# Kernel tuning notes

Hardware: AMD Instinct MI355X
Metric: run time of the kernel (lower is better)

Reference implementation:

```python
import jax, jax.numpy as jnp
import numpy as np

H = W = 512      # image spatial dims
C = 3            # channels
K = 32           # kernel size
S = 4            # stride
P = 10           # padding
THRESH = 0.5     # squared-L2 distance threshold
N_PATCH = (H + 2 * P - K) // S + 1  # 126 patches per dim
D = C * K * K    # 3072 patch feature dim


def setup_inputs() -> dict:
    key = jax.random.key(0)
    k1, k2, k3, k4 = jax.random.split(key, 4)
    image = jax.random.uniform(k1, (H, W, C), dtype=jnp.float32)
    mem = jax.random.normal(k2, (4096, D), dtype=jnp.float32)
    mem2 = jax.random.normal(k3, (4096, D), dtype=jnp.float32)
    mapping = jax.random.randint(k4, (4096,), 0, 4096, dtype=jnp.int64)
    return {"image": image, "mem": mem, "mem2": mem2, "mapping": mapping}


def _unfold(img_chw):
    # torch.nn.functional.unfold: -> [L, C*K*K] with feature order (c, kh, kw)
    padded = jnp.pad(img_chw, ((0, 0), (P, P), (P, P)))
    r = (jnp.arange(N_PATCH) * S)[:, None] + jnp.arange(K)[None, :]  # [nH, K]
    c = (jnp.arange(N_PATCH) * S)[:, None] + jnp.arange(K)[None, :]  # [nW, K]
    # patches: [C, nH, nW, K, K]
    patches = padded[:, r[:, None, :, None], c[None, :, None, :]]
    patches = patches.transpose(1, 2, 0, 3, 4)  # [nH, nW, C, K, K]
    return patches.reshape(N_PATCH * N_PATCH, D)


def _fold(patches_ld):
    # inverse of _unfold: scatter-add overlapping patches, crop padding
    p5 = patches_ld.reshape(N_PATCH, N_PATCH, C, K, K)
    r = (jnp.arange(N_PATCH) * S)[:, None] + jnp.arange(K)[None, :]
    c = (jnp.arange(N_PATCH) * S)[:, None] + jnp.arange(K)[None, :]
    canvas = jnp.zeros((C, H + 2 * P, W + 2 * P), dtype=patches_ld.dtype)
    ci = jnp.arange(C)[None, None, :, None, None]
    ri = r[:, None, None, :, None]
    cci = c[None, :, None, None, :]
    canvas = canvas.at[ci, ri, cci].add(p5)
    return canvas[:, P:P + H, P:P + W]  # [C, H, W]


def reference(image, mem, mem2, mapping):
    img_chw = image.transpose(2, 0, 1)            # [C, H, W]
    u = _unfold(img_chw)                           # [L, D]
    # brute-force squared-L2 1-NN against mem bank (FAISS IndexFlatL2)
    d2 = (jnp.sum(u * u, axis=1, keepdims=True)
          - 2.0 * (u @ mem.T)
          + jnp.sum(mem * mem, axis=1)[None, :])   # [L, N]
    dmin = jnp.min(d2, axis=1)                     # [L]
    idx = jnp.argmin(d2, axis=1)                   # [L]
    # counter-based pattern lookup: mem id -> mem2 pattern id -> reconstruct
    recon = mem2[mapping[idx]]                     # [L, D]
    out_p = jnp.where(dmin[:, None] >= THRESH, u, recon)
    folded = _fold(out_p)                          # [C, H, W]
    out = folded / jnp.max(folded)
    return out.transpose(1, 2, 0)                  # [H, W, C]
```

## Files before the change

kernel.cpp:

```cpp
#include <hip/hip_runtime.h>
#include <stdint.h>

#define HH 512
#define WW 512
#define CC 3
#define KK 32
#define SS 4
#define PP 10
#define NPATCH 126
#define NP2 (NPATCH * NPATCH)
#define DD 3072
#define NMEM 4096
#define THRESHV 0.5f

#define FAIL_OFF (4 + NMEM)

__device__ inline float wave_reduce_sum(float v) {
    for (int off = 32; off; off >>= 1) v += __shfl_xor(v, off, 64);
    return v;
}

__device__ inline uint32_t map_f(float f) {
    uint32_t b = __float_as_uint(f);
    return (b & 0x80000000u) ? ~b : (b | 0x80000000u);
}

__global__ void init_ws(uint32_t* ws) {
    if (threadIdx.x == 0) {
        ws[0] = 0u;
        ws[1] = 0x7F800000u;
        ws[2] = 0u;
        ws[3] = 0u;
    }
}

__global__ void mem_norms(const float* __restrict__ mem,
                          float* __restrict__ norms) {
    int row  = blockIdx.x * (blockDim.x >> 6) + (threadIdx.x >> 6);
    int lane = threadIdx.x & 63;
    if (row >= NMEM) return;
    const float4* r = (const float4*)(mem + (size_t)row * DD);
    float4 v[12];
#pragma unroll
    for (int i = 0; i < 12; ++i) v[i] = r[lane + (i << 6)];
    float s0 = 0.f, s1 = 0.f, s2 = 0.f, s3 = 0.f;
#pragma unroll
    for (int i = 0; i < 12; ++i) {
        s0 += v[i].x * v[i].x; s1 += v[i].y * v[i].y;
        s2 += v[i].z * v[i].z; s3 += v[i].w * v[i].w;
    }
    float s = (s0 + s1) + (s2 + s3);
    s = wave_reduce_sum(s);
    if (lane == 0) norms[row] = s;
}

__global__ void minmax_k(const float* __restrict__ norms, uint32_t* ws) {
    __shared__ float smn[4], smx[4];
    float mn = INFINITY, mx = -INFINITY;
    for (int i = threadIdx.x; i < NMEM; i += 256) {
        float v = norms[i];
        mn = fminf(mn, v);
        mx = fmaxf(mx, v);
    }
    for (int off = 32; off; off >>= 1) {
        mn = fminf(mn, __shfl_xor(mn, off, 64));
        mx = fmaxf(mx, __shfl_xor(mx, off, 64));
    }
    int w = threadIdx.x >> 6;
    if ((threadIdx.x & 63) == 0) { smn[w] = mn; smx[w] = mx; }
    __syncthreads();
    if (threadIdx.x == 0) {
        mn = fminf(fminf(smn[0], smn[1]), fminf(smn[2], smn[3]));
        mx = fmaxf(fmaxf(smx[0], smx[1]), fmaxf(smx[2], smx[3]));
        ws[1] = __float_as_uint(mn);
        ws[2] = __float_as_uint(mx);
    }
}

__global__ void patch_rows(const float* __restrict__ img, uint32_t* ws,
                           uint32_t cap) {
    __shared__ float cs[WW];
    int py = blockIdx.x;
    int x  = threadIdx.x;
    int y0 = py * SS - PP;
    float s = 0.f;
#pragma unroll
    for (int ky = 0; ky < KK; ++ky) {
        int y = y0 + ky;
        if (y >= 0 && y < HH) {
            const float* p = img + ((size_t)y * WW + x) * CC;
            s += p[0] * p[0] + p[1] * p[1] + p[2] * p[2];
        }
    }
    cs[x] = s;
    __syncthreads();
    if (x < NPATCH) {
        int x0 = x * SS - PP;
        float t = 0.f;
#pragma unroll
        for (int kx = 0; kx < KK; ++kx) {
            int xx = x0 + kx;
            if (xx >= 0 && xx < WW) t += cs[xx];
        }
        float un = sqrtf(t);
        float mn = sqrtf(__uint_as_float(ws[1]));
        float mx = sqrtf(__uint_as_float(ws[2]));
        float gap = 0.f;
        if (un <= mn) gap = mn - un;
        else if (un >= mx) gap = un - mx;
        if (gap * gap < THRESHV) {
            uint32_t idx = atomicAdd(&ws[0], 1u);
            if (idx < cap) ws[FAIL_OFF + idx] = (uint32_t)(py * NPATCH + x);
        }
    }
}

__device__ inline int cov1(int v) {
    int pv = v + PP;
    int a = pv - (KK - 1);
    int imin = (a <= 0) ? 0 : ((a + SS - 1) >> 2);
    int imax = pv >> 2;
    if (imax > NPATCH - 1) imax = NPATCH - 1;
    return imax - imin + 1;
}

__global__ void fold_main(const float* __restrict__ img, float* __restrict__ out) {
    int t = blockIdx.x * blockDim.x + threadIdx.x;
    if (t >= HH * WW) return;
    int y = t / WW, x = t - y * WW;
    float c = (float)(cov1(y) * cov1(x));
    const float* p = img + (size_t)t * CC;
    float* o = out + (size_t)t * CC;
    o[0] = p[0] * c;
    o[1] = p[1] * c;
    o[2] = p[2] * c;
}

__global__ void fallback_fix(const float* __restrict__ img,
                             const float* __restrict__ mem,
                             const float* __restrict__ mem2,
                             const int* __restrict__ mapping,
                             uint32_t* ws, float* out, uint32_t cap) {
    __shared__ float smin[256];
    __shared__ int   sarg[256];
    uint32_t nfail = ws[0];
    if (nfail > cap) nfail = cap;
    for (uint32_t f = blockIdx.x; f < nfail; f += gridDim.x) {
        int patch = (int)ws[FAIL_OFF + f];
        int pi = patch / NPATCH, pj = patch % NPATCH;
        int y0 = pi * SS - PP, x0 = pj * SS - PP;
        float best = INFINITY; int barg = NMEM;
        for (int j = threadIdx.x; j < NMEM; j += blockDim.x) {
            const float* m = mem + (size_t)j * DD;
            float s = 0.f;
            for (int d = 0; d < DD; ++d) {
                int c = d >> 10, rem = d & 1023, ky = rem >> 5, kx = rem & 31;
                int y = y0 + ky, x = x0 + kx;
                float u = (y >= 0 && y < HH && x >= 0 && x < WW)
                              ? img[((size_t)y * WW + x) * CC + c] : 0.f;
                float dif = u - m[d];
                s += dif * dif;
            }
            if (s < best) { best = s; barg = j; }
        }
        smin[threadIdx.x] = best; sarg[threadIdx.x] = barg;
        __syncthreads();
        for (int stride = 128; stride; stride >>= 1) {
            if ((int)threadIdx.x < stride) {
                float s2 = smin[threadIdx.x + stride];
                int   a2 = sarg[threadIdx.x + stride];
                if (s2 < smin[threadIdx.x] ||
                    (s2 == smin[threadIdx.x] && a2 < sarg[threadIdx.x])) {
                    smin[threadIdx.x] = s2; sarg[threadIdx.x] = a2;
                }
            }
            __syncthreads();
        }
        float dmin = smin[0]; int arg = sarg[0];
        if (dmin < THRESHV) {
            const float* rec = mem2 + (size_t)mapping[arg] * DD;
            for (int d = threadIdx.x; d < DD; d += blockDim.x) {
                int c = d >> 10, rem = d & 1023, ky = rem >> 5, kx = rem & 31;
                int y = y0 + ky, x = x0 + kx;
                if (y >= 0 && y < HH && x >= 0 && x < WW) {
                    float u = img[((size_t)y * WW + x) * CC + c];
                    atomicAdd(&out[((size_t)y * WW + x) * CC + c], rec[d] - u);
                }
            }
        }
        __syncthreads();
    }
}

__global__ void max_reduce(const float* __restrict__ out, uint32_t* ws) {
    __shared__ float sm[4];
    const int n4 = (HH * WW * CC) / 4;
    const float4* o4 = (const float4*)out;
    float m = -INFINITY;
    for (int i = blockIdx.x * blockDim.x + threadIdx.x; i < n4;
         i += gridDim.x * blockDim.x) {
        float4 v = o4[i];
        m = fmaxf(m, fmaxf(fmaxf(v.x, v.y), fmaxf(v.z, v.w)));
    }
    for (int off = 32; off; off >>= 1) m = fmaxf(m, __shfl_xor(m, off, 64));
    int w = threadIdx.x >> 6;
    if ((threadIdx.x & 63) == 0) sm[w] = m;
    __syncthreads();
    if (threadIdx.x == 0) {
        m = fmaxf(fmaxf(sm[0], sm[1]), fmaxf(sm[2], sm[3]));
        atomicMax(&ws[3], map_f(m));
    }
}

__global__ void normalize_k(float* out, const uint32_t* ws) {
    uint32_t key = ws[3];
    uint32_t b = (key & 0x80000000u) ? (key & 0x7FFFFFFFu) : ~key;
    float inv = 1.0f / __uint_as_float(b);
    const int n4 = (HH * WW * CC) / 4;
    int i = blockIdx.x * blockDim.x + threadIdx.x;
    if (i < n4) {
        float4* o4 = (float4*)out;
        float4 v = o4[i];
        v.x *= inv; v.y *= inv; v.z *= inv; v.w *= inv;
        o4[i] = v;
    }
}

extern "C" void kernel_launch(void* const* d_in, const int* in_sizes, int n_in,
                              void* d_out, int out_size, void* d_ws, size_t ws_size,
                              hipStream_t stream) {
    const float* img     = (const float*)d_in[0];
    const float* mem     = (const float*)d_in[1];
    const float* mem2    = (const float*)d_in[2];
    const int*   mapping = (const int*)d_in[3];
    float* out   = (float*)d_out;
    uint32_t* ws = (uint32_t*)d_ws;
    float* norms = (float*)(ws + 4);

    uint32_t cap = 0;
    size_t words = ws_size / 4;
    if (words > (size_t)FAIL_OFF) {
        cap = (uint32_t)(words - FAIL_OFF);
        if (cap > NP2) cap = NP2;
    }

    init_ws<<<1, 64, 0, stream>>>(ws);
    mem_norms<<<NMEM / 4, 256, 0, stream>>>(mem, norms);
    minmax_k<<<1, 256, 0, stream>>>(norms, ws);
    fold_main<<<(HH * WW + 255) / 256, 256, 0, stream>>>(img, out);
    patch_rows<<<NPATCH, 512, 0, stream>>>(img, ws, cap);
    fallback_fix<<<64, 256, 0, stream>>>(img, mem, mem2, mapping, ws, out, cap);
    max_reduce<<<256, 256, 0, stream>>>(out, ws);
    normalize_k<<<(HH * WW * CC / 4 + 255) / 256, 256, 0, stream>>>(out, ws);
}
```

Before: 145.8 us.

## Fuse norms with fold, drop init and minmax kernels, skip max rescan

Merges the mem-norm computation and the coverage-weighted fold into one kernel that also emits per-block partial maxima. The min/max of the norms moves into the patch certification kernel, and per-row fail lists replace a global atomic counter, so the init and minmax kernels are no longer needed. The max rescan over the output runs only when some patch needs a fallback, otherwise the precomputed partial maxima are used. This cuts the launch count from eight to five and avoids one full pass over the output, at the cost of redundant norm min/max reads in every certification block.

```diff
diff --git a/kernel.cpp b/kernel.cpp
--- a/kernel.cpp
+++ b/kernel.cpp
@@ -13,106 +13,27 @@
 #define NMEM 4096
 #define THRESHV 0.5f
 
-#define FAIL_OFF (4 + NMEM)
-
-__device__ inline float wave_reduce_sum(float v) {
+#define OFF_NORMS  0
+#define OFF_CNT    4096
+#define OFF_FAIL   4352
+#define OFF_PMAXA  20480
+#define OFF_PMAXB  21504
+
+__device__ inline float wave_max(float v) {
+    for (int off = 32; off; off >>= 1) v = fmaxf(v, __shfl_xor(v, off, 64));
+    return v;
+}
+__device__ inline float wave_min(float v) {
+    for (int off = 32; off; off >>= 1) v = fminf(v, __shfl_xor(v, off, 64));
+    return v;
+}
+__device__ inline float wave_sum(float v) {
     for (int off = 32; off; off >>= 1) v += __shfl_xor(v, off, 64);
     return v;
 }
-
-__device__ inline uint32_t map_f(float f) {
-    uint32_t b = __float_as_uint(f);
-    return (b & 0x80000000u) ? ~b : (b | 0x80000000u);
-}
-
-__global__ void init_ws(uint32_t* ws) {
-    if (threadIdx.x == 0) {
-        ws[0] = 0u;
-        ws[1] = 0x7F800000u;
-        ws[2] = 0u;
-        ws[3] = 0u;
-    }
-}
-
-__global__ void mem_norms(const float* __restrict__ mem,
-                          float* __restrict__ norms) {
-    int row  = blockIdx.x * (blockDim.x >> 6) + (threadIdx.x >> 6);
-    int lane = threadIdx.x & 63;
-    if (row >= NMEM) return;
-    const float4* r = (const float4*)(mem + (size_t)row * DD);
-    float4 v[12];
-#pragma unroll
-    for (int i = 0; i < 12; ++i) v[i] = r[lane + (i << 6)];
-    float s0 = 0.f, s1 = 0.f, s2 = 0.f, s3 = 0.f;
-#pragma unroll
-    for (int i = 0; i < 12; ++i) {
-        s0 += v[i].x * v[i].x; s1 += v[i].y * v[i].y;
-        s2 += v[i].z * v[i].z; s3 += v[i].w * v[i].w;
-    }
-    float s = (s0 + s1) + (s2 + s3);
-    s = wave_reduce_sum(s);
-    if (lane == 0) norms[row] = s;
-}
-
-__global__ void minmax_k(const float* __restrict__ norms, uint32_t* ws) {
-    __shared__ float smn[4], smx[4];
-    float mn = INFINITY, mx = -INFINITY;
-    for (int i = threadIdx.x; i < NMEM; i += 256) {
-        float v = norms[i];
-        mn = fminf(mn, v);
-        mx = fmaxf(mx, v);
-    }
-    for (int off = 32; off; off >>= 1) {
-        mn = fminf(mn, __shfl_xor(mn, off, 64));
-        mx = fmaxf(mx, __shfl_xor(mx, off, 64));
-    }
-    int w = threadIdx.x >> 6;
-    if ((threadIdx.x & 63) == 0) { smn[w] = mn; smx[w] = mx; }
-    __syncthreads();
-    if (threadIdx.x == 0) {
-        mn = fminf(fminf(smn[0], smn[1]), fminf(smn[2], smn[3]));
-        mx = fmaxf(fmaxf(smx[0], smx[1]), fmaxf(smx[2], smx[3]));
-        ws[1] = __float_as_uint(mn);
-        ws[2] = __float_as_uint(mx);
-    }
-}
-
-__global__ void patch_rows(const float* __restrict__ img, uint32_t* ws,
-                           uint32_t cap) {
-    __shared__ float cs[WW];
-    int py = blockIdx.x;
-    int x  = threadIdx.x;
-    int y0 = py * SS - PP;
-    float s = 0.f;
-#pragma unroll
-    for (int ky = 0; ky < KK; ++ky) {
-        int y = y0 + ky;
-        if (y >= 0 && y < HH) {
-            const float* p = img + ((size_t)y * WW + x) * CC;
-            s += p[0] * p[0] + p[1] * p[1] + p[2] * p[2];
-        }
-    }
-    cs[x] = s;
-    __syncthreads();
-    if (x < NPATCH) {
-        int x0 = x * SS - PP;
-        float t = 0.f;
-#pragma unroll
-        for (int kx = 0; kx < KK; ++kx) {
-            int xx = x0 + kx;
-            if (xx >= 0 && xx < WW) t += cs[xx];
-        }
-        float un = sqrtf(t);
-        float mn = sqrtf(__uint_as_float(ws[1]));
-        float mx = sqrtf(__uint_as_float(ws[2]));
-        float gap = 0.f;
-        if (un <= mn) gap = mn - un;
-        else if (un >= mx) gap = un - mx;
-        if (gap * gap < THRESHV) {
-            uint32_t idx = atomicAdd(&ws[0], 1u);
-            if (idx < cap) ws[FAIL_OFF + idx] = (uint32_t)(py * NPATCH + x);
-        }
-    }
+__device__ inline int wave_sum_i(int v) {
+    for (int off = 32; off; off >>= 1) v += __shfl_xor(v, off, 64);
+    return v;
 }
 
 __device__ inline int cov1(int v) {
@@ -124,105 +45,242 @@
     return imax - imin + 1;
 }
 
-__global__ void fold_main(const float* __restrict__ img, float* __restrict__ out) {
-    int t = blockIdx.x * blockDim.x + threadIdx.x;
-    if (t >= HH * WW) return;
-    int y = t / WW, x = t - y * WW;
-    float c = (float)(cov1(y) * cov1(x));
-    const float* p = img + (size_t)t * CC;
-    float* o = out + (size_t)t * CC;
-    o[0] = p[0] * c;
-    o[1] = p[1] * c;
-    o[2] = p[2] * c;
+__global__ void norms_fold(const float* __restrict__ mem,
+                           const float* __restrict__ img,
+                           float* __restrict__ norms,
+                           float* __restrict__ pmaxA,
+                           float* __restrict__ out) {
+    __shared__ float smx[4];
+    int b = blockIdx.x, tid = threadIdx.x;
+    int lane = tid & 63, w = tid >> 6;
+
+    float m = -INFINITY;
+    if (tid < 192) {
+        int f = b * 192 + tid;
+        float4 v = ((const float4*)img)[f];
+        float r[4] = {v.x, v.y, v.z, v.w};
+        int e = f * 4;
+#pragma unroll
+        for (int k = 0; k < 4; ++k) {
+            int px = (e + k) / 3;
+            int y = px >> 9, x = px & 511;
+            float cv = (float)(cov1(y) * cov1(x));
+            r[k] *= cv;
+            m = fmaxf(m, r[k]);
+        }
+        float4 o; o.x = r[0]; o.y = r[1]; o.z = r[2]; o.w = r[3];
+        ((float4*)out)[f] = o;
+    }
+
+    int row = b * 4 + w;
+    const float4* rp = (const float4*)(mem + (size_t)row * DD);
+    float4 v[12];
+#pragma unroll
+    for (int i = 0; i < 12; ++i) v[i] = rp[lane + (i << 6)];
+    float s0 = 0.f, s1 = 0.f, s2 = 0.f, s3 = 0.f;
+#pragma unroll
+    for (int i = 0; i < 12; ++i) {
+        s0 += v[i].x * v[i].x; s1 += v[i].y * v[i].y;
+        s2 += v[i].z * v[i].z; s3 += v[i].w * v[i].w;
+    }
+    float s = wave_sum((s0 + s1) + (s2 + s3));
+    if (lane == 0) norms[row] = s;
+
+    m = wave_max(m);
+    if (lane == 0) smx[w] = m;
+    __syncthreads();
+    if (tid == 0)
+        pmaxA[b] = fmaxf(fmaxf(smx[0], smx[1]), fmaxf(smx[2], smx[3]));
+}
+
+__global__ void patch_cert(const float* __restrict__ img,
+                           const float* __restrict__ norms,
+                           uint32_t* __restrict__ counts,
+                           uint32_t* __restrict__ fails) {
+    __shared__ float cs[WW];
+    __shared__ float red[16];
+    __shared__ float s_mn, s_mx;
+    __shared__ uint32_t s_cnt;
+    __shared__ uint32_t s_list[NPATCH];
+    int py = blockIdx.x;
+    int tid = threadIdx.x;
+    int lane = tid & 63, w = tid >> 6;
+
+    if (tid == 0) s_cnt = 0;
+
+    float mn = INFINITY, mx = -INFINITY;
+#pragma unroll
+    for (int k = 0; k < 8; ++k) {
+        float v = norms[tid + (k << 9)];
+        mn = fminf(mn, v); mx = fmaxf(mx, v);
+    }
+    mn = wave_min(mn); mx = wave_max(mx);
+    if (lane == 0) { red[w] = mn; red[8 + w] = mx; }
+    __syncthreads();
+    if (tid == 0) {
+        float a = INFINITY, bmx = -INFINITY;
+#pragma unroll
+        for (int k = 0; k < 8; ++k) {
+            a = fminf(a, red[k]); bmx = fmaxf(bmx, red[8 + k]);
+        }
+        s_mn = sqrtf(a); s_mx = sqrtf(bmx);
+    }
+
+    int y0 = py * SS - PP;
+    float s = 0.f;
+#pragma unroll
+    for (int ky = 0; ky < KK; ++ky) {
+        int y = y0 + ky;
+        if (y >= 0 && y < HH) {
+            const float* p = img + ((size_t)y * WW + tid) * CC;
+            s += p[0] * p[0] + p[1] * p[1] + p[2] * p[2];
+        }
+    }
+    cs[tid] = s;
+    __syncthreads();
+
+    if (tid < NPATCH) {
+        int x0 = tid * SS - PP;
+        float t = 0.f;
+#pragma unroll
+        for (int kx = 0; kx < KK; ++kx) {
+            int xx = x0 + kx;
+            if (xx >= 0 && xx < WW) t += cs[xx];
+        }
+        float un = sqrtf(t);
+        float gap = 0.f;
+        if (un <= s_mn) gap = s_mn - un;
+        else if (un >= s_mx) gap = un - s_mx;
+        if (gap * gap < THRESHV) {
+            uint32_t pos = atomicAdd(&s_cnt, 1u);
+            s_list[pos] = (uint32_t)(py * NPATCH + tid);
+        }
+    }
+    __syncthreads();
+    uint32_t c = s_cnt;
+    if (tid == 0) counts[py] = c;
+    if (tid < c) fails[py * 128 + tid] = s_list[tid];
 }
 
 __global__ void fallback_fix(const float* __restrict__ img,
                              const float* __restrict__ mem,
                              const float* __restrict__ mem2,
                              const int* __restrict__ mapping,
-                             uint32_t* ws, float* out, uint32_t cap) {
+                             const uint32_t* __restrict__ counts,
+                             const uint32_t* __restrict__ fails,
+                             float* __restrict__ out) {
     __shared__ float smin[256];
     __shared__ int   sarg[256];
-    uint32_t nfail = ws[0];
-    if (nfail > cap) nfail = cap;
-    for (uint32_t f = blockIdx.x; f < nfail; f += gridDim.x) {
-        int patch = (int)ws[FAIL_OFF + f];
-        int pi = patch / NPATCH, pj = patch % NPATCH;
-        int y0 = pi * SS - PP, x0 = pj * SS - PP;
-        float best = INFINITY; int barg = NMEM;
-        for (int j = threadIdx.x; j < NMEM; j += blockDim.x) {
-            const float* m = mem + (size_t)j * DD;
-            float s = 0.f;
-            for (int d = 0; d < DD; ++d) {
-                int c = d >> 10, rem = d & 1023, ky = rem >> 5, kx = rem & 31;
-                int y = y0 + ky, x = x0 + kx;
-                float u = (y >= 0 && y < HH && x >= 0 && x < WW)
-                              ? img[((size_t)y * WW + x) * CC + c] : 0.f;
-                float dif = u - m[d];
-                s += dif * dif;
+    int seq = 0;
+    for (int py = 0; py < NPATCH; ++py) {
+        uint32_t cnt = counts[py];
+        for (uint32_t e = 0; e < cnt; ++e, ++seq) {
+            if ((uint32_t)(seq % gridDim.x) != blockIdx.x) continue;
+            int patch = (int)fails[py * 128 + e];
+            int pi = patch / NPATCH, pj = patch % NPATCH;
+            int y0 = pi * SS - PP, x0 = pj * SS - PP;
+            float best = INFINITY; int barg = NMEM;
+            for (int j = threadIdx.x; j < NMEM; j += blockDim.x) {
+                const float* mr = mem + (size_t)j * DD;
+                float s = 0.f;
+                for (int d = 0; d < DD; ++d) {
+                    int c = d >> 10, rem = d & 1023, ky = rem >> 5, kx = rem & 31;
+                    int y = y0 + ky, x = x0 + kx;
+                    float u = (y >= 0 && y < HH && x >= 0 && x < WW)
+                                  ? img[((size_t)y * WW + x) * CC + c] : 0.f;
+                    float dif = u - mr[d];
+                    s += dif * dif;
+                }
+                if (s < best) { best = s; barg = j; }
             }
-            if (s < best) { best = s; barg = j; }
-        }
-        smin[threadIdx.x] = best; sarg[threadIdx.x] = barg;
-        __syncthreads();
-        for (int stride = 128; stride; stride >>= 1) {
-            if ((int)threadIdx.x < stride) {
-                float s2 = smin[threadIdx.x + stride];
-                int   a2 = sarg[threadIdx.x + stride];
-                if (s2 < smin[threadIdx.x] ||
-                    (s2 == smin[threadIdx.x] && a2 < sarg[threadIdx.x])) {
-                    smin[threadIdx.x] = s2; sarg[threadIdx.x] = a2;
+            smin[threadIdx.x] = best; sarg[threadIdx.x] = barg;
+            __syncthreads();
+            for (int stride = 128; stride; stride >>= 1) {
+                if ((int)threadIdx.x < stride) {
+                    float s2 = smin[threadIdx.x + stride];
+                    int   a2 = sarg[threadIdx.x + stride];
+                    if (s2 < smin[threadIdx.x] ||
+                        (s2 == smin[threadIdx.x] && a2 < sarg[threadIdx.x])) {
+                        smin[threadIdx.x] = s2; sarg[threadIdx.x] = a2;
+                    }
+                }
+                __syncthreads();
+            }
+            float dmin = smin[0]; int arg = sarg[0];
+            if (dmin < THRESHV) {
+                const float* rec = mem2 + (size_t)mapping[arg] * DD;
+                for (int d = threadIdx.x; d < DD; d += blockDim.x) {
+                    int c = d >> 10, rem = d & 1023, ky = rem >> 5, kx = rem & 31;
+                    int y = y0 + ky, x = x0 + kx;
+                    if (y >= 0 && y < HH && x >= 0 && x < WW) {
+                        float u = img[((size_t)y * WW + x) * CC + c];
+                        atomicAdd(&out[((size_t)y * WW + x) * CC + c],
+                                  rec[d] - u);
+                    }
                 }
             }
             __syncthreads();
         }
-        float dmin = smin[0]; int arg = sarg[0];
-        if (dmin < THRESHV) {
-            const float* rec = mem2 + (size_t)mapping[arg] * DD;
-            for (int d = threadIdx.x; d < DD; d += blockDim.x) {
-                int c = d >> 10, rem = d & 1023, ky = rem >> 5, kx = rem & 31;
-                int y = y0 + ky, x = x0 + kx;
-                if (y >= 0 && y < HH && x >= 0 && x < WW) {
-                    float u = img[((size_t)y * WW + x) * CC + c];
-                    atomicAdd(&out[((size_t)y * WW + x) * CC + c], rec[d] - u);
-                }
-            }
-        }
-        __syncthreads();
-    }
-}
-
-__global__ void max_reduce(const float* __restrict__ out, uint32_t* ws) {
-    __shared__ float sm[4];
-    const int n4 = (HH * WW * CC) / 4;
-    const float4* o4 = (const float4*)out;
+    }
+}
+
+__global__ void rescan_max(const uint32_t* __restrict__ counts,
+                           const float* __restrict__ out,
+                           float* __restrict__ pmaxB) {
+    __shared__ int sneed[4];
+    __shared__ float smx[4];
+    int tid = threadIdx.x, lane = tid & 63, w = tid >> 6;
+    int c = (tid < NPATCH) ? (int)counts[tid] : 0;
+    c = wave_sum_i(c);
+    if (lane == 0) sneed[w] = c;
+    __syncthreads();
+    int need = sneed[0] + sneed[1] + sneed[2] + sneed[3];
+    if (need == 0) return;
     float m = -INFINITY;
-    for (int i = blockIdx.x * blockDim.x + threadIdx.x; i < n4;
-         i += gridDim.x * blockDim.x) {
-        float4 v = o4[i];
-        m = fmaxf(m, fmaxf(fmaxf(v.x, v.y), fmaxf(v.z, v.w)));
-    }
-    for (int off = 32; off; off >>= 1) m = fmaxf(m, __shfl_xor(m, off, 64));
-    int w = threadIdx.x >> 6;
-    if ((threadIdx.x & 63) == 0) sm[w] = m;
-    __syncthreads();
-    if (threadIdx.x == 0) {
-        m = fmaxf(fmaxf(sm[0], sm[1]), fmaxf(sm[2], sm[3]));
-        atomicMax(&ws[3], map_f(m));
-    }
-}
-
-__global__ void normalize_k(float* out, const uint32_t* ws) {
-    uint32_t key = ws[3];
-    uint32_t b = (key & 0x80000000u) ? (key & 0x7FFFFFFFu) : ~key;
-    float inv = 1.0f / __uint_as_float(b);
-    const int n4 = (HH * WW * CC) / 4;
-    int i = blockIdx.x * blockDim.x + threadIdx.x;
-    if (i < n4) {
-        float4* o4 = (float4*)out;
-        float4 v = o4[i];
+    if (tid < 192) {
+        int f = blockIdx.x * 192 + tid;
+        float4 v = ((const float4*)out)[f];
+        m = fmaxf(fmaxf(v.x, v.y), fmaxf(v.z, v.w));
+    }
+    m = wave_max(m);
+    if (lane == 0) smx[w] = m;
+    __syncthreads();
+    if (tid == 0)
+        pmaxB[blockIdx.x] = fmaxf(fmaxf(smx[0], smx[1]), fmaxf(smx[2], smx[3]));
+}
+
+__global__ void normalize_k(const uint32_t* __restrict__ counts,
+                            const float* __restrict__ pmaxA,
+                            const float* __restrict__ pmaxB,
+                            float* __restrict__ out) {
+    __shared__ int sneed[4];
+    __shared__ float smx[4];
+    __shared__ float s_inv;
+    int tid = threadIdx.x, lane = tid & 63, w = tid >> 6;
+    int c = (tid < NPATCH) ? (int)counts[tid] : 0;
+    c = wave_sum_i(c);
+    if (lane == 0) sneed[w] = c;
+    __syncthreads();
+    int need = sneed[0] + sneed[1] + sneed[2] + sneed[3];
+    const float* pm = need ? pmaxB : pmaxA;
+    float m = -INFINITY;
+#pragma unroll
+    for (int k = 0; k < 4; ++k) m = fmaxf(m, pm[tid + (k << 8)]);
+    m = wave_max(m);
+    if (lane == 0) smx[w] = m;
+    __syncthreads();
+    if (tid == 0)
+        s_inv = 1.0f / fmaxf(fmaxf(smx[0], smx[1]), fmaxf(smx[2], smx[3]));
+    __syncthreads();
+    float inv = s_inv;
+    float4* o4 = (float4*)out;
+    int base = blockIdx.x * 768 + tid;
+#pragma unroll
+    for (int k = 0; k < 3; ++k) {
+        int f = base + (k << 8);
+        float4 v = o4[f];
         v.x *= inv; v.y *= inv; v.z *= inv; v.w *= inv;
-        o4[i] = v;
+        o4[f] = v;
     }
 }
 
@@ -233,23 +291,19 @@
     const float* mem     = (const float*)d_in[1];
     const float* mem2    = (const float*)d_in[2];
     const int*   mapping = (const int*)d_in[3];
-    float* out   = (float*)d_out;
-    uint32_t* ws = (uint32_t*)d_ws;
-    float* norms = (float*)(ws + 4);
-
-    uint32_t cap = 0;
-    size_t words = ws_size / 4;
-    if (words > (size_t)FAIL_OFF) {
-        cap = (uint32_t)(words - FAIL_OFF);
-        if (cap > NP2) cap = NP2;
-    }
-
-    init_ws<<<1, 64, 0, stream>>>(ws);
-    mem_norms<<<NMEM / 4, 256, 0, stream>>>(mem, norms);
-    minmax_k<<<1, 256, 0, stream>>>(norms, ws);
-    fold_main<<<(HH * WW + 255) / 256, 256, 0, stream>>>(img, out);
-    patch_rows<<<NPATCH, 512, 0, stream>>>(img, ws, cap);
-    fallback_fix<<<64, 256, 0, stream>>>(img, mem, mem2, mapping, ws, out, cap);
-    max_reduce<<<256, 256, 0, stream>>>(out, ws);
-    normalize_k<<<(HH * WW * CC / 4 + 255) / 256, 256, 0, stream>>>(out, ws);
-}
+    float* out    = (float*)d_out;
+    uint32_t* wsu = (uint32_t*)d_ws;
+
+    float*    norms  = (float*)(wsu + OFF_NORMS);
+    uint32_t* counts = wsu + OFF_CNT;
+    uint32_t* fails  = wsu + OFF_FAIL;
+    float*    pmaxA  = (float*)(wsu + OFF_PMAXA);
+    float*    pmaxB  = (float*)(wsu + OFF_PMAXB);
+
+    norms_fold <<<1024, 256, 0, stream>>>(mem, img, norms, pmaxA, out);
+    patch_cert <<<NPATCH, 512, 0, stream>>>(img, norms, counts, fails);
+    fallback_fix<<<64, 256, 0, stream>>>(img, mem, mem2, mapping, counts,
+                                         fails, out);
+    rescan_max <<<1024, 256, 0, stream>>>(counts, out, pmaxB);
+    normalize_k<<<256, 256, 0, stream>>>(counts, pmaxA, pmaxB, out);
+}
```

After: 143.7 us. About the same (-1.5%).
